# Optimization experiments

Measured on AMD Instinct MI355X. Metric: run time of the kernel, lower is better.

## Reference

```python
import jax, jax.numpy as jnp
import numpy as np

SEQ, BATCH = 512, 32
VOCAB, HID, FF = 32000, 1024, 4096
HEADS, NX, MAXLEN = 8, 6, 512
EPS = 1e-5


def _full_layer_norm(t):
    # F.layer_norm(t, t.shape): normalize over ALL elements, no affine
    m = jnp.mean(t)
    v = jnp.mean((t - m) ** 2)
    return (t - m) * jax.lax.rsqrt(v + EPS)


def _attention(x, wq, bq, wk, bk, wv, bv, wo, bo):
    # x: [S, B, H]; faithful to the module's quirky reshape:
    # view(B, S//heads, heads, H) splits the SEQUENCE dim across heads,
    # each head keeps the full feature dim H; scores scaled by sqrt(H//heads).
    S, B, H = x.shape
    head_dim = H // HEADS
    q = x @ wq + bq
    k = x @ wk + bk
    v = x @ wv + bv

    def split(t):  # [S,B,H] -> [B, heads, S//heads, H]
        return t.transpose(1, 0, 2).reshape(B, S // HEADS, HEADS, H).transpose(0, 2, 1, 3)

    qh, kh, vh = split(q), split(k), split(v)
    energy = jnp.einsum('bhtf,bhsf->bhts', qh, kh) / np.sqrt(head_dim)
    att = jax.nn.softmax(energy, axis=-1)          # [B, heads, S//h, S//h]
    va = jnp.einsum('bhts,bhsf->bhtf', att, vh)    # [B, heads, S//h, H]
    va = va.transpose(2, 0, 1, 3).reshape(S, B, H)  # back to [S, B, H]
    return va @ wo + bo


def _sub_encoder(x, p, i):
    a = _attention(x, p['wq'][i], p['bq'][i], p['wk'][i], p['bk'][i],
                   p['wv'][i], p['bv'][i], p['wo'][i], p['bo'][i])
    mid = _full_layer_norm(a + x)
    f = jax.nn.relu(mid @ p['w1'][i] + p['b1'][i]) @ p['w2'][i] + p['b2'][i]
    return _full_layer_norm(mid + f)


def setup_inputs() -> dict:
    key = jax.random.key(0)
    ks = jax.random.split(key, 16)
    s = 0.02
    inp = {
        'x': jax.random.randint(ks[0], (SEQ, BATCH), 0, VOCAB),
        'emb': jax.random.normal(ks[1], (VOCAB, HID), jnp.float32) * s,
        'pos_emb': jax.random.normal(ks[2], (MAXLEN, HID), jnp.float32) * s,
        'wq': jax.random.normal(ks[3], (NX, HID, HID), jnp.float32) * s,
        'bq': jnp.zeros((NX, HID), jnp.float32),
        'wk': jax.random.normal(ks[4], (NX, HID, HID), jnp.float32) * s,
        'bk': jnp.zeros((NX, HID), jnp.float32),
        'wv': jax.random.normal(ks[5], (NX, HID, HID), jnp.float32) * s,
        'bv': jnp.zeros((NX, HID), jnp.float32),
        'wo': jax.random.normal(ks[6], (NX, HID, HID), jnp.float32) * s,
        'bo': jnp.zeros((NX, HID), jnp.float32),
        'w1': jax.random.normal(ks[7], (NX, HID, FF), jnp.float32) * s,
        'b1': jnp.zeros((NX, FF), jnp.float32),
        'w2': jax.random.normal(ks[8], (NX, FF, HID), jnp.float32) * s,
        'b2': jnp.zeros((NX, HID), jnp.float32),
    }
    return inp


def reference(x, emb, pos_emb, wq, bq, wk, bk, wv, bv, wo, bo, w1, b1, w2, b2):
    # dropout layers are identity (eval mode); src_mask=None path
    S = x.shape[0]
    p = dict(wq=wq, bq=bq, wk=wk, bk=bk, wv=wv, bv=bv, wo=wo, bo=bo,
             w1=w1, b1=b1, w2=w2, b2=b2)
    h = emb[x] * np.sqrt(HID) + pos_emb[jnp.arange(S)][:, None, :]
    for i in range(NX):
        h = _sub_encoder(h, p, i)
    return h
```

## Files before the change

### kernel.cpp

```cpp
#include <hip/hip_runtime.h>
#include <hip/hip_bf16.h>
#include <stdint.h>

typedef __bf16 bf16_t;
typedef __bf16 bf16x8 __attribute__((ext_vector_type(8)));
typedef __bf16 bf16x4 __attribute__((ext_vector_type(4)));
typedef float  f32x4  __attribute__((ext_vector_type(4)));
typedef float  f32x16 __attribute__((ext_vector_type(16)));

#define SEQ   512
#define BATCH 32
#define HID   1024
#define FFD   4096
#define NROW  (SEQ*BATCH)
#define NTOT  ((long)NROW*HID)
#define QKVS  3072

typedef __attribute__((address_space(3))) uint32_t lds_u32;
typedef __attribute__((address_space(1))) const uint32_t glb_u32;

__device__ __forceinline__ void gload_lds16(const void* g, void* l) {
  glb_u32* gp = reinterpret_cast<glb_u32*>(reinterpret_cast<uintptr_t>(g));
  lds_u32* lp = reinterpret_cast<lds_u32*>(reinterpret_cast<uintptr_t>(l));
  __builtin_amdgcn_global_load_lds(gp, lp, 16, 0, 0);
}
#define BAR() asm volatile("s_barrier" ::: "memory")

__global__ __launch_bounds__(256) void embed_k(const int* __restrict__ x,
    const float* __restrict__ emb, const float* __restrict__ pos,
    bf16_t* __restrict__ hb)
{
  const long row = blockIdx.x;
  const int  s   = (int)(row >> 5);
  const long idx = x[row];
  const int  t   = threadIdx.x;
  float4 e  = ((const float4*)(emb + idx*HID))[t];
  float4 pv = ((const float4*)(pos + (long)s*HID))[t];
  bf16x4 ob = {(bf16_t)(e.x*32.f+pv.x), (bf16_t)(e.y*32.f+pv.y),
               (bf16_t)(e.z*32.f+pv.z), (bf16_t)(e.w*32.f+pv.w)};
  *(bf16x4*)(hb + row*HID + (long)t*4) = ob;
}

__device__ __forceinline__ void stats_reduce(const float* __restrict__ part,
    int np, double* shd, float& mS, float& rS, int nthr)
{
  if (np == 0) { mS = 0.f; rS = 1.f; return; }
  const int tid = threadIdx.x;
  double s = 0.0, s2 = 0.0;
  for (int i = tid; i < np; i += nthr) { s += (double)part[2*i]; s2 += (double)part[2*i+1]; }
#pragma unroll
  for (int o = 1; o < 64; o <<= 1) { s += __shfl_xor(s, o); s2 += __shfl_xor(s2, o); }
  __syncthreads();
  const int w = tid >> 6, nw = nthr >> 6;
  if ((tid & 63) == 0) { shd[w] = s; shd[8 + w] = s2; }
  __syncthreads();
  double ts = 0.0, ts2 = 0.0;
  for (int i = 0; i < nw; ++i) { ts += shd[i]; ts2 += shd[8 + i]; }
  const double mean = ts / (double)NTOT;
  const double var  = ts2 / (double)NTOT - mean*mean;
  mS = (float)mean;
  rS = (float)(1.0 / sqrt(var + 1e-5));
}

__device__ __forceinline__ void wcvtNL_body(const float* __restrict__ W,
    bf16_t* __restrict__ wT, int K, int N, int bid)
{
  const int t  = threadIdx.x;
  const int nt = N >> 9;
  const int n  = ((bid % nt) << 9) + t;
  const int k0 = (bid / nt) << 6;
#pragma unroll
  for (int kb = 0; kb < 64; kb += 8) {
    bf16x8 o;
#pragma unroll
    for (int j = 0; j < 8; ++j)
      o[j] = (bf16_t)W[(long)(k0 + kb + j)*N + n];
    *(bf16x8*)&wT[(long)n*K + k0 + kb] = o;
  }
}

__device__ __forceinline__ void csum512_body(const float* __restrict__ W,
    float* __restrict__ out, int K, int N, int bid)
{
  const int n = bid*512 + threadIdx.x;
  float s0 = 0.f, s1 = 0.f, s2 = 0.f, s3 = 0.f;
  for (int k = 0; k < K; k += 4) {
    s0 += W[(long)k*N + n];
    s1 += W[(long)(k+1)*N + n];
    s2 += W[(long)(k+2)*N + n];
    s3 += W[(long)(k+3)*N + n];
  }
  out[n] = (s0 + s1) + (s2 + s3);
}

__global__ __launch_bounds__(512) void prep0(const float* __restrict__ wq,
    const float* __restrict__ wk, const float* __restrict__ wv,
    bf16_t* __restrict__ wT3, float* __restrict__ cs3)
{
  const int b = blockIdx.x;
  if (b < 96) {
    const int sel = b >> 5;
    const float* W = sel == 0 ? wq : sel == 1 ? wk : wv;
    wcvtNL_body(W, wT3 + (size_t)sel*HID*HID, HID, HID, b & 31);
  } else {
    const int col = (b - 96)*512 + threadIdx.x;
    const int sel = col >> 10, n = col & 1023;
    const float* W = sel == 0 ? wq : sel == 1 ? wk : wv;
    float s = 0.f;
    for (int k = 0; k < HID; ++k) s += W[(long)k*HID + n];
    cs3[col] = s;
  }
}

__global__ __launch_bounds__(512) void prep_k(
    const float* __restrict__ Wo, bf16_t* __restrict__ wTo,
    const float* __restrict__ W1, bf16_t* __restrict__ wT1, float* __restrict__ cs1,
    const float* __restrict__ W2, bf16_t* __restrict__ wT2,
    const float* __restrict__ Wq, const float* __restrict__ Wk,
    const float* __restrict__ Wv, bf16_t* __restrict__ wT3,
    float* __restrict__ cs3)
{
  const int b = blockIdx.x;
  if (b < 32)        wcvtNL_body(Wo, wTo, HID, HID, b);
  else if (b < 160)  wcvtNL_body(W1, wT1, HID, FFD, b - 32);
  else if (b < 288)  wcvtNL_body(W2, wT2, FFD, HID, b - 160);
  else if (b < 296)  csum512_body(W1, cs1, HID, FFD, b - 288);
  else if (b < 392) {
    const int i = b - 296, sel = i >> 5;
    const float* W = sel == 0 ? Wq : sel == 1 ? Wk : Wv;
    wcvtNL_body(W, wT3 + (size_t)sel*HID*HID, HID, HID, i & 31);
  } else {
    const int col = (b - 392)*512 + threadIdx.x;
    const int sel = col >> 10, n = col & 1023;
    const float* W = sel == 0 ? Wq : sel == 1 ? Wk : Wv;
    float s = 0.f;
    for (int k = 0; k < HID; ++k) s += W[(long)k*HID + n];
    cs3[col] = s;
  }
}

template<int MODE>
__global__ __launch_bounds__(512, 4)
void gemmW(const bf16_t* __restrict__ A, const bf16_t* __restrict__ Bt,
           const float* __restrict__ ba, const float* __restrict__ bb,
           const float* __restrict__ bc, const float* __restrict__ cs,
           const float* __restrict__ partIn, int npIn,
           const bf16_t* __restrict__ res,
           bf16_t* __restrict__ outB, float* __restrict__ part,
           int M, int N, int K)
{
  __shared__ bf16_t As[128][64];
  __shared__ bf16_t Bs[256][64];
  __shared__ float  rs[512], rq[512];
  const int tid = threadIdx.x;
  const int w = tid >> 6, l = tid & 63;
  const int wm = w >> 2, wn = w & 3;
  const int lr = l & 31, hi = l >> 5;

  const int nbn = N >> 8;
  const int nwg = gridDim.x;
  const int q8 = nwg >> 3, r8 = nwg & 7;
  const int xcd = blockIdx.x & 7, bidx = blockIdx.x >> 3;
  const int wg = (xcd < r8 ? xcd*(q8+1) : r8*(q8+1) + (xcd-r8)*q8) + bidx;
  const long bm = wg / nbn, bn = wg % nbn;
  const long rA0 = bm << 7, rB0 = bn << 8;

  const int srow   = tid >> 3;
  const int schunk = (((tid & 7) ^ ((tid >> 3) & 7)) << 3);
  const int ldsw   = (tid >> 6) << 10;

  f32x16 a00 = {0}, a01 = {0}, a10 = {0}, a11 = {0};

#define STG_TILE(kt) do { \
    const long kb_ = (long)(kt)*64 + schunk; \
    gload_lds16(A  + (rA0 + srow)*(long)K + kb_,        (char*)As + ldsw); \
    gload_lds16(A  + (rA0 + 64 + srow)*(long)K + kb_,   (char*)As + 8192 + ldsw); \
    gload_lds16(Bt + (rB0 + srow)*(long)K + kb_,        (char*)Bs + ldsw); \
    gload_lds16(Bt + (rB0 + 64 + srow)*(long)K + kb_,   (char*)Bs + 8192 + ldsw); \
    gload_lds16(Bt + (rB0 + 128 + srow)*(long)K + kb_,  (char*)Bs + 16384 + ldsw); \
    gload_lds16(Bt + (rB0 + 192 + srow)*(long)K + kb_,  (char*)Bs + 24576 + ldsw); \
  } while (0)
#define FRA(mt, kk) (*(const bf16x8*)((const char*)As + (wm*64 + (mt)*32 + lr)*128 + \
                      ((((kk)*2 + hi) ^ (l & 7)) << 4)))
#define FRB(nt, kk) (*(const bf16x8*)((const char*)Bs + (wn*64 + (nt)*32 + lr)*128 + \
                      ((((kk)*2 + hi) ^ (l & 7)) << 4)))

  const int nk = K >> 6;
  for (int t = 0; t < nk; ++t) {
    __syncthreads();
    STG_TILE(t);
    __syncthreads();
#pragma unroll
    for (int kk = 0; kk < 4; ++kk) {
      bf16x8 fa0 = FRA(0, kk), fa1 = FRA(1, kk);
      bf16x8 fb0 = FRB(0, kk), fb1 = FRB(1, kk);
      a00 = __builtin_amdgcn_mfma_f32_32x32x16_bf16(fa0, fb0, a00, 0, 0, 0);
      a01 = __builtin_amdgcn_mfma_f32_32x32x16_bf16(fa0, fb1, a01, 0, 0, 0);
      a10 = __builtin_amdgcn_mfma_f32_32x32x16_bf16(fa1, fb0, a10, 0, 0, 0);
      a11 = __builtin_amdgcn_mfma_f32_32x32x16_bf16(fa1, fb1, a11, 0, 0, 0);
    }
  }
#undef STG_TILE
#undef FRA
#undef FRB

  float mS, rS;
  stats_reduce(partIn, npIn, (double*)&As[0][0], mS, rS, 512);

  const bool q3 = (N == 3072);
  float ls = 0.f, lsq = 0.f;
  const long rowT = rA0 + wm*64 + 4*hi;
  const long colT = rB0 + wn*64 + lr;
#pragma unroll
  for (int nt = 0; nt < 2; ++nt) {
    const long col = colT + nt*32;
    float bv;
    if (MODE == 3 && q3)
      bv = col < 1024 ? ba[col] : col < 2048 ? bb[col - 1024] : bc[col - 2048];
    else
      bv = ba[col];
    float beta = 0.f;
    if (MODE == 3 || MODE == 4) beta = bv - mS*rS*cs[col];
#pragma unroll
    for (int mt = 0; mt < 2; ++mt) {
      const f32x16 acc = mt == 0 ? (nt == 0 ? a00 : a01) : (nt == 0 ? a10 : a11);
#pragma unroll
      for (int r = 0; r < 16; ++r) {
        const long row = rowT + mt*32 + (r & 3) + 8*(r >> 2);
        const long off = row*(long)N + col;
        float v;
        if (MODE == 3)      v = fmaf(acc[r], rS, beta);
        else if (MODE == 4) v = fmaxf(fmaf(acc[r], rS, beta), 0.f);
        else {
          v = acc[r] + bv + ((float)res[off] - mS)*rS;
          ls += v; lsq += v*v;
        }
        outB[off] = (bf16_t)v;
      }
    }
  }
  if (MODE == 5) {
    rs[tid] = ls; rq[tid] = lsq;
    __syncthreads();
    for (int o = 256; o > 0; o >>= 1) {
      if (tid < o) { rs[tid] += rs[tid+o]; rq[tid] += rq[tid+o]; }
      __syncthreads();
    }
    if (tid == 0) { part[2*blockIdx.x] = rs[0]; part[2*blockIdx.x + 1] = rq[0]; }
  }
}

__global__ __launch_bounds__(256) void attn_m(
    const bf16_t* __restrict__ qkv, bf16_t* __restrict__ ob)
{
  __shared__ __align__(16) bf16_t Qb[2][8192];
  __shared__ __align__(16) bf16_t Kb[2][8192];
  __shared__ __align__(16) bf16_t Ps[4096];
  bf16_t* Vs = &Qb[0][0];
  bf16_t* Os = &Kb[0][0];

  const int tid = threadIdx.x;
  const int w = tid >> 6, l = tid & 63;
  const int fr = l & 15, kq = l >> 4;
  const int head = blockIdx.x & 7, b = blockIdx.x >> 3;
  const long rbase = (long)head*32 + b;

  const int lr  = tid >> 2;
  const int sslot = (tid & 15) ^ (tid >> 4);

  f32x4 accS[4] = {{0,0,0,0},{0,0,0,0},{0,0,0,0},{0,0,0,0}};

#define STAGE_QK(qb, kb, kc) do { \
    _Pragma("unroll") for (int i_ = 0; i_ < 4; ++i_) { \
      const int r_ = i_*16 + (tid >> 4); \
      const long gq_ = ((long)r_*256 + rbase)*QKVS + (kc) + sslot*8; \
      gload_lds16(qkv + gq_,        (char*)(qb) + i_*4096 + w*1024); \
      gload_lds16(qkv + gq_ + 1024, (char*)(kb) + i_*4096 + w*1024); \
    } } while (0)

  STAGE_QK(Qb[0], Kb[0], 0);
#pragma unroll
  for (int c = 0; c < 8; ++c) {
    const int cur = c & 1;
    if (c < 7) {
      STAGE_QK(Qb[cur ^ 1], Kb[cur ^ 1], (c + 1)*128);
      asm volatile("s_waitcnt vmcnt(8)" ::: "memory");
    } else {
      asm volatile("s_waitcnt vmcnt(0)" ::: "memory");
    }
    BAR();
#pragma unroll
    for (int kk = 0; kk < 4; ++kk) {
      const int ra = w*16 + fr;
      bf16x8 a = *(const bf16x8*)&Qb[cur][ra*128 + (((kk*4 + kq) ^ fr) << 3)];
#pragma unroll
      for (int n = 0; n < 4; ++n) {
        const int rb = n*16 + fr;
        bf16x8 bv = *(const bf16x8*)&Kb[cur][rb*128 + (((kk*4 + kq) ^ fr) << 3)];
        accS[n] = __builtin_amdgcn_mfma_f32_16x16x32_bf16(a, bv, accS[n], 0, 0, 0);
      }
    }
    BAR();
  }
#undef STAGE_QK

  const float scale = 0.08838834764831843f;
  float pj[4][4];
#pragma unroll
  for (int j = 0; j < 4; ++j) {
    float m = fmaxf(fmaxf(accS[0][j], accS[1][j]), fmaxf(accS[2][j], accS[3][j]));
    m = fmaxf(m, __shfl_xor(m, 1));
    m = fmaxf(m, __shfl_xor(m, 2));
    m = fmaxf(m, __shfl_xor(m, 4));
    m = fmaxf(m, __shfl_xor(m, 8));
    m *= scale;
    float s = 0.f;
#pragma unroll
    for (int n = 0; n < 4; ++n) { pj[n][j] = __expf(accS[n][j]*scale - m); s += pj[n][j]; }
    s += __shfl_xor(s, 1);
    s += __shfl_xor(s, 2);
    s += __shfl_xor(s, 4);
    s += __shfl_xor(s, 8);
    const float rv = 1.f / s;
#pragma unroll
    for (int n = 0; n < 4; ++n) pj[n][j] *= rv;
  }
#pragma unroll
  for (int n = 0; n < 4; ++n)
#pragma unroll
    for (int j = 0; j < 4; ++j) {
      const int r = w*16 + kq*4 + j;
      const int cpos = n*16 + fr;
      Ps[r*64 + (((cpos >> 3) ^ (r & 7)) << 3) + (cpos & 7)] = (bf16_t)pj[n][j];
    }
  __syncthreads();

  const long orow = (long)lr*256 + b*8 + head;
  const bf16_t* vbase = qkv + ((long)lr*256 + rbase)*QKVS + 2048;
  const int ra2 = w*16 + fr;
  bf16x8 a0 = *(const bf16x8*)&Ps[ra2*64 + ((kq       ^ (ra2 & 7)) << 3)];
  bf16x8 a1 = *(const bf16x8*)&Ps[ra2*64 + (((4 + kq) ^ (ra2 & 7)) << 3)];

  uint4 vr[4];
#pragma unroll
  for (int i = 0; i < 4; ++i)
    vr[i] = *(const uint4*)&vbase[(tid & 3)*8 + i*32];

#pragma unroll
  for (int fc8 = 0; fc8 < 8; ++fc8) {
#pragma unroll
    for (int i = 0; i < 4; ++i) {
      const int f0 = (tid & 3)*8 + i*32;
      const bf16_t* ve = (const bf16_t*)&vr[i];
#pragma unroll
      for (int j = 0; j < 8; ++j) {
        const int f = f0 + j;
        Vs[f*64 + (((lr >> 3) ^ (f & 7)) << 3) + (lr & 7)] = ve[j];
      }
    }
    __syncthreads();
    if (fc8 < 7) {
#pragma unroll
      for (int i = 0; i < 4; ++i)
        vr[i] = *(const uint4*)&vbase[(fc8 + 1)*128 + (tid & 3)*8 + i*32];
    }
    f32x4 accO[8];
#pragma unroll
    for (int nt = 0; nt < 8; ++nt) {
      const int f = nt*16 + fr;
      bf16x8 b0 = *(const bf16x8*)&Vs[f*64 + ((kq       ^ (f & 7)) << 3)];
      bf16x8 b1 = *(const bf16x8*)&Vs[f*64 + (((4 + kq) ^ (f & 7)) << 3)];
      accO[nt] = __builtin_amdgcn_mfma_f32_16x16x32_bf16(a0, b0, (f32x4){0.f,0.f,0.f,0.f}, 0, 0, 0);
      accO[nt] = __builtin_amdgcn_mfma_f32_16x16x32_bf16(a1, b1, accO[nt], 0, 0, 0);
    }
#pragma unroll
    for (int nt = 0; nt < 8; ++nt)
#pragma unroll
      for (int j = 0; j < 4; ++j) {
        const int r = w*16 + kq*4 + j;
        const int cpos = nt*16 + fr;
        Os[r*128 + (((cpos >> 3) ^ (r & 7)) << 3) + (cpos & 7)] = (bf16_t)accO[nt][j];
      }
    __syncthreads();
#pragma unroll
    for (int i = 0; i < 4; ++i) {
      const int p = (tid & 3)*4 + i;
      uint4 vv = *(const uint4*)&Os[lr*128 + ((p ^ (lr & 7)) << 3)];
      *(uint4*)&ob[orow*HID + fc8*128 + p*8] = vv;
    }
  }
}

__global__ __launch_bounds__(256) void final_norm(const bf16_t* __restrict__ t,
    const float* __restrict__ part, int np, float* __restrict__ out)
{
  __shared__ double shd[16];
  float m, r;
  stats_reduce(part, np, shd, m, r, 256);
  const long n8 = NTOT / 8;
  for (long i = (long)blockIdx.x*blockDim.x + threadIdx.x; i < n8;
       i += (long)gridDim.x*blockDim.x) {
    bf16x8 v = ((const bf16x8*)t)[i];
    float4 o0 = {((float)v[0]-m)*r, ((float)v[1]-m)*r, ((float)v[2]-m)*r, ((float)v[3]-m)*r};
    float4 o1 = {((float)v[4]-m)*r, ((float)v[5]-m)*r, ((float)v[6]-m)*r, ((float)v[7]-m)*r};
    ((float4*)out)[2*i]   = o0;
    ((float4*)out)[2*i+1] = o1;
  }
}

extern "C" void kernel_launch(void* const* d_in, const int* in_sizes, int n_in,
                              void* d_out, int out_size, void* d_ws, size_t ws_size,
                              hipStream_t stream)
{
  const int*   x    = (const int*)  d_in[0];
  const float* emb  = (const float*)d_in[1];
  const float* pos  = (const float*)d_in[2];
  const float* wq_a = (const float*)d_in[3];
  const float* bq_a = (const float*)d_in[4];
  const float* wk_a = (const float*)d_in[5];
  const float* bk_a = (const float*)d_in[6];
  const float* wv_a = (const float*)d_in[7];
  const float* bv_a = (const float*)d_in[8];
  const float* wo_a = (const float*)d_in[9];
  const float* bo_a = (const float*)d_in[10];
  const float* w1_a = (const float*)d_in[11];
  const float* b1_a = (const float*)d_in[12];
  const float* w2_a = (const float*)d_in[13];
  const float* b2_a = (const float*)d_in[14];

  char* p = (char*)d_ws;
  auto take = [&](size_t n) { char* r = p; p += (n + 255) & ~(size_t)255; return r; };
  bf16_t* hb   = (bf16_t*)take(NTOT*2);
  bf16_t* U    = (bf16_t*)take((size_t)NROW*FFD*2);
  bf16_t* qkv  = U;
  bf16_t* attb = U + 3*NTOT;
  bf16_t* ffb  = U;
  bf16_t* wTo  = (bf16_t*)take((size_t)HID*HID*2);
  bf16_t* wT1  = (bf16_t*)take((size_t)HID*FFD*2);
  bf16_t* wT2  = (bf16_t*)take((size_t)HID*FFD*2);
  bf16_t* wT3  = (bf16_t*)take((size_t)3*HID*HID*2);
  float*  cs1  = (float*) take(FFD*4);
  float*  cs3  = (float*) take(QKVS*4);
  float*  part1= (float*) take(2048*4);
  float*  part2= (float*) take(2048*4);

  const int gQKV = (NROW/128)*(QKVS/256);
  const int gH   = (NROW/128)*(HID/256);
  const int gF   = (NROW/128)*(FFD/256);

  embed_k<<<NROW, 256, 0, stream>>>(x, emb, pos, hb);
  prep0<<<102, 512, 0, stream>>>(wq_a, wk_a, wv_a, wT3, cs3);

  for (int i = 0; i < 6; ++i) {
    const float* Bq = bq_a + (size_t)i*HID;
    const float* Bk = bk_a + (size_t)i*HID;
    const float* Bv = bv_a + (size_t)i*HID;
    const float* Wo = wo_a + (size_t)i*HID*HID;  const float* Bo = bo_a + (size_t)i*HID;
    const float* W1 = w1_a + (size_t)i*HID*FFD;  const float* B1 = b1_a + (size_t)i*FFD;
    const float* W2 = w2_a + (size_t)i*FFD*HID;  const float* B2 = b2_a + (size_t)i*HID;
    const int npIn = (i == 0) ? 0 : gH;
    const int haveNext = (i < 5);
    const float* Wqn = wq_a + (size_t)(i+1)*HID*HID;
    const float* Wkn = wk_a + (size_t)(i+1)*HID*HID;
    const float* Wvn = wv_a + (size_t)(i+1)*HID*HID;

    gemmW<3><<<gQKV, 512, 0, stream>>>(hb, wT3, Bq, Bk, Bv, cs3, part2, npIn,
                                       nullptr, qkv, nullptr, NROW, QKVS, HID);

    attn_m<<<256, 256, 0, stream>>>(qkv, attb);

    prep_k<<<haveNext ? 398 : 296, 512, 0, stream>>>(
        Wo, wTo, W1, wT1, cs1, W2, wT2, Wqn, Wkn, Wvn, wT3, cs3);

    gemmW<5><<<gH, 512, 0, stream>>>(attb, wTo, Bo, Bo, Bo, nullptr, part2, npIn,
                                     hb, hb, part1, NROW, HID, HID);

    gemmW<4><<<gF, 512, 0, stream>>>(hb, wT1, B1, B1, B1, cs1, part1, gH,
                                     nullptr, ffb, nullptr, NROW, FFD, HID);

    gemmW<5><<<gH, 512, 0, stream>>>(ffb, wT2, B2, B2, B2, nullptr, part1, gH,
                                     hb, hb, part2, NROW, HID, FFD);
  }

  final_norm<<<2048, 256, 0, stream>>>(hb, part2, gH, (float*)d_out);
}
```

Before: 3.405 ms.

## Double attention block size to 512 threads, splitting score columns and output features

```diff
diff --git a/kernel.cpp b/kernel.cpp
--- a/kernel.cpp
+++ b/kernel.cpp
@@ -250,32 +250,32 @@
   }
 }
 
-__global__ __launch_bounds__(256) void attn_m(
+__global__ __launch_bounds__(512) void attn_m(
     const bf16_t* __restrict__ qkv, bf16_t* __restrict__ ob)
 {
   __shared__ __align__(16) bf16_t Qb[2][8192];
   __shared__ __align__(16) bf16_t Kb[2][8192];
   __shared__ __align__(16) bf16_t Ps[4096];
+  __shared__ float Sx[128];
   bf16_t* Vs = &Qb[0][0];
   bf16_t* Os = &Kb[0][0];
 
   const int tid = threadIdx.x;
   const int w = tid >> 6, l = tid & 63;
   const int fr = l & 15, kq = l >> 4;
+  const int rt = w & 3, ch = w >> 2;
   const int head = blockIdx.x & 7, b = blockIdx.x >> 3;
   const long rbase = (long)head*32 + b;
 
-  const int lr  = tid >> 2;
-  const int sslot = (tid & 15) ^ (tid >> 4);
-
-  f32x4 accS[4] = {{0,0,0,0},{0,0,0,0},{0,0,0,0},{0,0,0,0}};
+  f32x4 accS[2] = {{0,0,0,0},{0,0,0,0}};
 
 #define STAGE_QK(qb, kb, kc) do { \
-    _Pragma("unroll") for (int i_ = 0; i_ < 4; ++i_) { \
-      const int r_ = i_*16 + (tid >> 4); \
-      const long gq_ = ((long)r_*256 + rbase)*QKVS + (kc) + sslot*8; \
-      gload_lds16(qkv + gq_,        (char*)(qb) + i_*4096 + w*1024); \
-      gload_lds16(qkv + gq_ + 1024, (char*)(kb) + i_*4096 + w*1024); \
+    _Pragma("unroll") for (int i_ = 0; i_ < 2; ++i_) { \
+      const int row_ = i_*32 + w*4 + (l >> 4); \
+      const int c16_ = (l & 15) ^ (row_ & 15); \
+      const long gq_ = ((long)row_*256 + rbase)*QKVS + (kc) + c16_*8; \
+      gload_lds16(qkv + gq_,        (char*)(qb) + i_*8192 + w*1024); \
+      gload_lds16(qkv + gq_ + 1024, (char*)(kb) + i_*8192 + w*1024); \
     } } while (0)
 
   STAGE_QK(Qb[0], Kb[0], 0);
@@ -284,18 +284,18 @@
     const int cur = c & 1;
     if (c < 7) {
       STAGE_QK(Qb[cur ^ 1], Kb[cur ^ 1], (c + 1)*128);
-      asm volatile("s_waitcnt vmcnt(8)" ::: "memory");
+      asm volatile("s_waitcnt vmcnt(4)" ::: "memory");
     } else {
       asm volatile("s_waitcnt vmcnt(0)" ::: "memory");
     }
     BAR();
+    const int ra = rt*16 + fr;
 #pragma unroll
     for (int kk = 0; kk < 4; ++kk) {
-      const int ra = w*16 + fr;
       bf16x8 a = *(const bf16x8*)&Qb[cur][ra*128 + (((kk*4 + kq) ^ fr) << 3)];
 #pragma unroll
-      for (int n = 0; n < 4; ++n) {
-        const int rb = n*16 + fr;
+      for (int n = 0; n < 2; ++n) {
+        const int rb = ch*32 + n*16 + fr;
         bf16x8 bv = *(const bf16x8*)&Kb[cur][rb*128 + (((kk*4 + kq) ^ fr) << 3)];
         accS[n] = __builtin_amdgcn_mfma_f32_16x16x32_bf16(a, bv, accS[n], 0, 0, 0);
       }
@@ -305,89 +305,107 @@
 #undef STAGE_QK
 
   const float scale = 0.08838834764831843f;
-  float pj[4][4];
+  float mrow[4], srow[4], pj[2][4];
 #pragma unroll
   for (int j = 0; j < 4; ++j) {
-    float m = fmaxf(fmaxf(accS[0][j], accS[1][j]), fmaxf(accS[2][j], accS[3][j]));
+    float m = fmaxf(accS[0][j], accS[1][j]);
     m = fmaxf(m, __shfl_xor(m, 1));
     m = fmaxf(m, __shfl_xor(m, 2));
     m = fmaxf(m, __shfl_xor(m, 4));
     m = fmaxf(m, __shfl_xor(m, 8));
-    m *= scale;
+    mrow[j] = m;
+    if (fr == j) Sx[(rt*16 + kq*4 + j)*2 + ch] = m;
+  }
+  __syncthreads();
+#pragma unroll
+  for (int j = 0; j < 4; ++j) {
+    const float m = fmaxf(mrow[j], Sx[(rt*16 + kq*4 + j)*2 + (ch ^ 1)]) * scale;
     float s = 0.f;
 #pragma unroll
-    for (int n = 0; n < 4; ++n) { pj[n][j] = __expf(accS[n][j]*scale - m); s += pj[n][j]; }
+    for (int n = 0; n < 2; ++n) { pj[n][j] = __expf(accS[n][j]*scale - m); s += pj[n][j]; }
     s += __shfl_xor(s, 1);
     s += __shfl_xor(s, 2);
     s += __shfl_xor(s, 4);
     s += __shfl_xor(s, 8);
-    const float rv = 1.f / s;
-#pragma unroll
-    for (int n = 0; n < 4; ++n) pj[n][j] *= rv;
-  }
-#pragma unroll
-  for (int n = 0; n < 4; ++n)
+    srow[j] = s;
+  }
+  __syncthreads();
+#pragma unroll
+  for (int j = 0; j < 4; ++j)
+    if (fr == j) Sx[(rt*16 + kq*4 + j)*2 + ch] = srow[j];
+  __syncthreads();
+#pragma unroll
+  for (int j = 0; j < 4; ++j) {
+    const float rv = 1.f / (srow[j] + Sx[(rt*16 + kq*4 + j)*2 + (ch ^ 1)]);
+#pragma unroll
+    for (int n = 0; n < 2; ++n) pj[n][j] *= rv;
+  }
+#pragma unroll
+  for (int n = 0; n < 2; ++n)
 #pragma unroll
     for (int j = 0; j < 4; ++j) {
-      const int r = w*16 + kq*4 + j;
-      const int cpos = n*16 + fr;
+      const int r = rt*16 + kq*4 + j;
+      const int cpos = ch*32 + n*16 + fr;
       Ps[r*64 + (((cpos >> 3) ^ (r & 7)) << 3) + (cpos & 7)] = (bf16_t)pj[n][j];
     }
   __syncthreads();
 
-  const long orow = (long)lr*256 + b*8 + head;
-  const bf16_t* vbase = qkv + ((long)lr*256 + rbase)*QKVS + 2048;
-  const int ra2 = w*16 + fr;
+  const int rt2 = w & 3, fh = w >> 2;
+  const int lr2 = tid >> 3;
+  const long orow = (long)lr2*256 + b*8 + head;
+  const bf16_t* vbase = qkv + ((long)lr2*256 + rbase)*QKVS + 2048;
+  const int ra2 = rt2*16 + fr;
   bf16x8 a0 = *(const bf16x8*)&Ps[ra2*64 + ((kq       ^ (ra2 & 7)) << 3)];
   bf16x8 a1 = *(const bf16x8*)&Ps[ra2*64 + (((4 + kq) ^ (ra2 & 7)) << 3)];
 
-  uint4 vr[4];
-#pragma unroll
-  for (int i = 0; i < 4; ++i)
-    vr[i] = *(const uint4*)&vbase[(tid & 3)*8 + i*32];
+  uint4 vr[2];
+#pragma unroll
+  for (int i = 0; i < 2; ++i)
+    vr[i] = *(const uint4*)&vbase[(tid & 7)*16 + i*8];
 
 #pragma unroll
   for (int fc8 = 0; fc8 < 8; ++fc8) {
 #pragma unroll
-    for (int i = 0; i < 4; ++i) {
-      const int f0 = (tid & 3)*8 + i*32;
+    for (int i = 0; i < 2; ++i) {
+      const int f0 = (tid & 7)*16 + i*8;
       const bf16_t* ve = (const bf16_t*)&vr[i];
 #pragma unroll
       for (int j = 0; j < 8; ++j) {
         const int f = f0 + j;
-        Vs[f*64 + (((lr >> 3) ^ (f & 7)) << 3) + (lr & 7)] = ve[j];
+        Vs[f*64 + (((lr2 >> 3) ^ (f & 7)) << 3) + (lr2 & 7)] = ve[j];
       }
     }
     __syncthreads();
     if (fc8 < 7) {
 #pragma unroll
-      for (int i = 0; i < 4; ++i)
-        vr[i] = *(const uint4*)&vbase[(fc8 + 1)*128 + (tid & 3)*8 + i*32];
-    }
-    f32x4 accO[8];
-#pragma unroll
-    for (int nt = 0; nt < 8; ++nt) {
-      const int f = nt*16 + fr;
+      for (int i = 0; i < 2; ++i)
+        vr[i] = *(const uint4*)&vbase[(fc8 + 1)*128 + (tid & 7)*16 + i*8];
+    }
+    f32x4 accO[4];
+#pragma unroll
+    for (int nt = 0; nt < 4; ++nt) {
+      const int f = fh*64 + nt*16 + fr;
       bf16x8 b0 = *(const bf16x8*)&Vs[f*64 + ((kq       ^ (f & 7)) << 3)];
       bf16x8 b1 = *(const bf16x8*)&Vs[f*64 + (((4 + kq) ^ (f & 7)) << 3)];
       accO[nt] = __builtin_amdgcn_mfma_f32_16x16x32_bf16(a0, b0, (f32x4){0.f,0.f,0.f,0.f}, 0, 0, 0);
       accO[nt] = __builtin_amdgcn_mfma_f32_16x16x32_bf16(a1, b1, accO[nt], 0, 0, 0);
     }
 #pragma unroll
-    for (int nt = 0; nt < 8; ++nt)
+    for (int nt = 0; nt < 4; ++nt)
 #pragma unroll
       for (int j = 0; j < 4; ++j) {
-        const int r = w*16 + kq*4 + j;
-        const int cpos = nt*16 + fr;
+        const int r = rt2*16 + kq*4 + j;
+        const int cpos = fh*64 + nt*16 + fr;
         Os[r*128 + (((cpos >> 3) ^ (r & 7)) << 3) + (cpos & 7)] = (bf16_t)accO[nt][j];
       }
     __syncthreads();
 #pragma unroll
-    for (int i = 0; i < 4; ++i) {
-      const int p = (tid & 3)*4 + i;
-      uint4 vv = *(const uint4*)&Os[lr*128 + ((p ^ (lr & 7)) << 3)];
+    for (int i = 0; i < 2; ++i) {
+      const int p = (tid & 7)*2 + i;
+      uint4 vv = *(const uint4*)&Os[lr2*128 + ((p ^ (lr2 & 7)) << 3)];
       *(uint4*)&ob[orow*HID + fc8*128 + p*8] = vv;
     }
+    __syncthreads();
   }
 }
 
@@ -467,7 +485,7 @@
     gemmW<3><<<gQKV, 512, 0, stream>>>(hb, wT3, Bq, Bk, Bv, cs3, part2, npIn,
                                        nullptr, qkv, nullptr, NROW, QKVS, HID);
 
-    attn_m<<<256, 256, 0, stream>>>(qkv, attb);
+    attn_m<<<256, 512, 0, stream>>>(qkv, attb);
 
     prep_k<<<haveNext ? 398 : 296, 512, 0, stream>>>(
         Wo, wTo, W1, wT1, cs1, W2, wT2, Wqn, Wkn, Wvn, wT3, cs3);
```

After: 3.429 ms. Within noise of the previous version (+0.7%).
